# Kernel optimization log

Hardware: AMD Instinct MI355X
Metric: run time of the kernel (lower is better)

Reference implementation:

```python
import jax, jax.numpy as jnp
import numpy as np

B, S = 2, 1024
NH, NKV, HD = 32, 8, 128
Q_DIM, KV_DIM = NH * HD, NKV * HD
LEVEL = 256
ROPE_BASE = 10000.0


def fq_sym(x, level=LEVEL):
    # symmetric per-tensor fake quant with straight-through estimator
    qp = level // 2 - 1
    s = jnp.maximum(jax.lax.stop_gradient(jnp.max(jnp.abs(x))) / qp, 1e-8)
    q = jnp.clip(jnp.round(x / s), -qp, qp) * s
    return x + jax.lax.stop_gradient(q - x)


def fq_asym(x, level=LEVEL):
    # asymmetric (unsigned) fake quant for values in [0, 1]
    qp = level - 1
    s = jnp.maximum(jax.lax.stop_gradient(jnp.max(x)) / qp, 1e-8)
    q = jnp.clip(jnp.round(x / s), 0, qp) * s
    return x + jax.lax.stop_gradient(q - x)


def rope_tables(seq_len, dim):
    inv_freq = 1.0 / (ROPE_BASE ** (jnp.arange(0, dim, 2, dtype=jnp.float32) / dim))
    freqs = jnp.arange(seq_len, dtype=jnp.float32)[:, None] * inv_freq[None, :]  # [S, HD/2]
    emb = jnp.concatenate([freqs, freqs], axis=-1)  # [S, HD]
    return jnp.cos(emb), jnp.sin(emb)


def rotate_half(x):
    x1, x2 = jnp.split(x, 2, axis=-1)
    return jnp.concatenate([-x2, x1], axis=-1)


def setup_inputs() -> dict:
    key = jax.random.key(0)
    k1, k2, k3, k4 = jax.random.split(key, 4)
    d = Q_DIM + 2 * KV_DIM
    x = jax.random.normal(k1, (B, S, d), dtype=jnp.float32)
    w_qkv = jax.random.normal(k2, (d, d), dtype=jnp.float32) * (d ** -0.5)
    w_o = jax.random.normal(k3, (Q_DIM, Q_DIM), dtype=jnp.float32) * (Q_DIM ** -0.5)
    core_slope = jnp.float32(0.25)
    causal_mask = jnp.where(
        jnp.triu(jnp.ones((S, S), dtype=bool), k=1), jnp.float32(-1e9), jnp.float32(0.0)
    )[None, None]
    return {"x": x, "w_qkv": w_qkv, "w_o": w_o, "core_slope": core_slope,
            "causal_mask": causal_mask}


def reference(x, w_qkv, w_o, core_slope, causal_mask):
    qkv = jnp.einsum("bsd,ed->bse", x, w_qkv)  # Linear, no bias
    q = qkv[..., :Q_DIM].reshape(B, S, NH, HD).transpose(0, 2, 1, 3)
    k = qkv[..., Q_DIM:Q_DIM + KV_DIM].reshape(B, S, NKV, HD).transpose(0, 2, 1, 3)
    v = qkv[..., Q_DIM + KV_DIM:].reshape(B, S, NKV, HD).transpose(0, 2, 1, 3)
    q, k, v = fq_sym(q), fq_sym(k), fq_sym(v)
    cos, sin = rope_tables(S, HD)
    cos, sin = cos[None, None], sin[None, None]  # [1,1,S,HD]
    q = q * cos + rotate_half(q) * sin
    k = k * cos + rotate_half(k) * sin
    groups = NH // NKV
    if groups > 1:
        k = jnp.repeat(k, groups, axis=1)  # [B,NH,S,HD]
        v = jnp.repeat(v, groups, axis=1)
    scale = HD ** -0.5
    scores = jnp.einsum("bhqd,bhkd->bhqk", q, k) * scale
    scores = scores + causal_mask
    attn = jnp.clip(0.5 + core_slope * scores, 0.0, 1.0)  # UniAffineCore -> [0,1]
    attn = fq_asym(attn)
    out = jnp.einsum("bhqk,bhkd->bhqd", attn, v)
    out = fq_sym(out)
    out = out.transpose(0, 2, 1, 3).reshape(B, S, Q_DIM)
    out = jnp.einsum("bsd,ed->bse", out, w_o)
    return fq_sym(out)
```

## Files before the change

### kernel.cpp

```cpp
#include <hip/hip_runtime.h>
#include <stdint.h>

#define BB   2
#define SS   1024
#define NH   32
#define NKV  8
#define HD   128
#define DQ   4096
#define DKV  1024
#define DD   6144
#define MM   2048
#define SCALE 0.08838834764831845f

typedef __attribute__((ext_vector_type(8))) short short8;
typedef __attribute__((ext_vector_type(4))) float f4;

__device__ __forceinline__ float b2f(unsigned short b) {
    union { unsigned int u; float f; } v; v.u = ((unsigned int)b) << 16; return v.f;
}
__device__ __forceinline__ unsigned short f2b(float f) {
    union { float f; unsigned int u; } v; v.f = f;
    unsigned int u = v.u;
    unsigned int r = u + 0x7fffu + ((u >> 16) & 1u);
    return (unsigned short)(r >> 16);
}
__device__ __forceinline__ float fqs(float x, float s) {
    return fminf(fmaxf(rintf(x / s), -127.f), 127.f) * s;
}

typedef const unsigned int __attribute__((address_space(1)))* gas_ptr;
typedef unsigned int __attribute__((address_space(3)))* las_ptr;
__device__ __forceinline__ void gl_lds16(const void* g, void* l) {
    __builtin_amdgcn_global_load_lds((gas_ptr)(uintptr_t)g,
                                     (las_ptr)(unsigned int)(uintptr_t)l, 16, 0, 0);
}

__global__ void detect_kernel(const unsigned short* __restrict__ x, float* scal) {
    __shared__ float w[4];
    int tid = threadIdx.x;
    float m = 0.f;
    for (int i = tid; i < 65536; i += 256) m = fmaxf(m, fabsf(b2f(x[i])));
#pragma unroll
    for (int off = 32; off > 0; off >>= 1) m = fmaxf(m, __shfl_down(m, off));
    if ((tid & 63) == 0) w[tid >> 6] = m;
    __syncthreads();
    if (tid == 0) {
        float mm = fmaxf(fmaxf(w[0], w[1]), fmaxf(w[2], w[3]));
        scal[6] = (mm > 1e4f) ? 1.0f : 0.0f;
    }
}

__global__ void slope_kernel(const unsigned short* __restrict__ sp, float* scal) {
    if (threadIdx.x == 0)
        scal[7] = (scal[6] > 0.5f) ? ((const float*)sp)[0] : b2f(sp[0]);
}

__global__ void convert_split_kernel(const unsigned short* __restrict__ src,
                                     unsigned short* __restrict__ hi,
                                     unsigned short* __restrict__ lo,
                                     const float* __restrict__ scal) {
    size_t t = (size_t)blockIdx.x * 256 + threadIdx.x;
    float v[8] __attribute__((aligned(16)));
    if (scal[6] > 0.5f) {
        const float* s = (const float*)src + t * 8;
        *(float4*)(v)     = *(const float4*)(s);
        *(float4*)(v + 4) = *(const float4*)(s + 4);
    } else {
        unsigned short u[8] __attribute__((aligned(16)));
        *(uint4*)u = *(const uint4*)(src + t * 8);
#pragma unroll
        for (int i = 0; i < 8; i++) v[i] = b2f(u[i]);
    }
    unsigned short h8[8] __attribute__((aligned(16)));
    unsigned short l8[8] __attribute__((aligned(16)));
#pragma unroll
    for (int i = 0; i < 8; i++) {
        unsigned short h = f2b(v[i]);
        h8[i] = h;
        l8[i] = f2b(v[i] - b2f(h));
    }
    *(uint4*)(hi + t * 8) = *(uint4*)h8;
    *(uint4*)(lo + t * 8) = *(uint4*)l8;
}

template<int NT, int MODE>
__global__ __launch_bounds__(256, 4)
void gemm_hilo_kernel(const unsigned short* __restrict__ Ah,
                      const unsigned short* __restrict__ Al,
                      const unsigned short* __restrict__ Bh,
                      const unsigned short* __restrict__ Bl,
                      float* __restrict__ C,
                      int M, int N, int K,
                      float* __restrict__ scal)
{
    constexpr int PA    = 128 * 32;
    constexpr int OAL   = PA;
    constexpr int OBH   = (NT == 3) ? 2 * PA : PA;
    constexpr int OBL   = OBH + PA;
    __shared__ unsigned short lds[OBL + PA];
    __shared__ float wred[4];

    const int tid = threadIdx.x;
    const int bn = blockIdx.x << 7;
    const int bm = blockIdx.y << 7;
    const int wave = tid >> 6, lane = tid & 63;
    const int wm = (wave >> 1) << 6, wn = (wave & 1) << 6;
    const int lm = lane & 15, quad = lane >> 4;
    const int qx = quad ^ ((lm >> 1) & 3);

    const f4 z = {0.f, 0.f, 0.f, 0.f};
    f4 acc[4][4];
#pragma unroll
    for (int i = 0; i < 4; i++)
#pragma unroll
        for (int j = 0; j < 4; j++) acc[i][j] = z;

    const int r0 = tid >> 2;
    const int cs = ((tid & 3) ^ ((r0 >> 1) & 3)) * 8;
    const size_t ra0 = (size_t)(bm + r0) * K + cs;
    const size_t ra1 = (size_t)(bm + r0 + 64) * K + cs;
    const size_t rb0 = (size_t)(bn + r0) * K + cs;
    const size_t rb1 = (size_t)(bn + r0 + 64) * K + cs;
    const int l0 = tid * 8, l1 = (tid + 256) * 8;

    for (int k0 = 0; k0 < K; k0 += 32) {
        gl_lds16(Ah + ra0 + k0, lds + l0);
        gl_lds16(Ah + ra1 + k0, lds + l1);
        if (NT == 3) {
            gl_lds16(Al + ra0 + k0, lds + OAL + l0);
            gl_lds16(Al + ra1 + k0, lds + OAL + l1);
        }
        gl_lds16(Bh + rb0 + k0, lds + OBH + l0);
        gl_lds16(Bh + rb1 + k0, lds + OBH + l1);
        gl_lds16(Bl + rb0 + k0, lds + OBL + l0);
        gl_lds16(Bl + rb1 + k0, lds + OBL + l1);
        __syncthreads();
        short8 a_h[4], b_h[4], b_l[4];
        short8 a_l[(NT == 3) ? 4 : 1];
#pragma unroll
        for (int t = 0; t < 4; t++) {
            int ro = (wm + t * 16 + lm) * 32 + qx * 8;
            a_h[t] = *(const short8*)(lds + ro);
            if (NT == 3) a_l[t] = *(const short8*)(lds + OAL + ro);
        }
#pragma unroll
        for (int t = 0; t < 4; t++) {
            int ro = (wn + t * 16 + lm) * 32 + qx * 8;
            b_h[t] = *(const short8*)(lds + OBH + ro);
            b_l[t] = *(const short8*)(lds + OBL + ro);
        }
#pragma unroll
        for (int i = 0; i < 4; i++)
#pragma unroll
            for (int j = 0; j < 4; j++) {
                acc[i][j] = __builtin_amdgcn_mfma_f32_16x16x32_bf16(a_h[i], b_h[j], acc[i][j], 0, 0, 0);
                if (NT == 3)
                    acc[i][j] = __builtin_amdgcn_mfma_f32_16x16x32_bf16(a_l[i], b_h[j], acc[i][j], 0, 0, 0);
                acc[i][j] = __builtin_amdgcn_mfma_f32_16x16x32_bf16(a_h[i], b_l[j], acc[i][j], 0, 0, 0);
            }
        __syncthreads();
    }

    float mult = 1.f;
    if (MODE == 1) mult = fmaxf(scal[4] / 127.f, 1e-8f);
    float amax = 0.f;
#pragma unroll
    for (int i = 0; i < 4; i++)
#pragma unroll
        for (int j = 0; j < 4; j++)
#pragma unroll
            for (int r = 0; r < 4; r++) {
                float v = acc[i][j][r] * mult;
                amax = fmaxf(amax, fabsf(v));
                size_t row = (size_t)(bm + wm + i * 16 + quad * 4 + r);
                size_t col = (size_t)(bn + wn + j * 16 + lm);
                C[row * (size_t)N + col] = v;
            }
#pragma unroll
    for (int off = 32; off > 0; off >>= 1) amax = fmaxf(amax, __shfl_down(amax, off));
    if (lane == 0) wred[wave] = amax;
    __syncthreads();
    if (tid == 0) {
        float m = fmaxf(fmaxf(wred[0], wred[1]), fmaxf(wred[2], wred[3]));
        int slot = (MODE == 0) ? ((bn < 4096) ? 0 : ((bn < 5120) ? 1 : 2)) : 5;
        atomicMax((unsigned int*)(scal + slot), __float_as_uint(m));
    }
}

__global__ void quant_rope_hilo_kernel(const float* __restrict__ qkv,
                                       unsigned short* __restrict__ Qh,
                                       unsigned short* __restrict__ Ql,
                                       unsigned short* __restrict__ Kh,
                                       unsigned short* __restrict__ Kl,
                                       unsigned short* __restrict__ Vc,
                                       const float* __restrict__ scal)
{
    int t = blockIdx.x * 256 + threadIdx.x;
    int f = t * 8;
    int r = f / DD;
    int c = f - r * DD;
    int b = r >> 10, sp = r & 1023;
    const float* src = qkv + (size_t)r * DD + c;
    float x[8] __attribute__((aligned(16)));
    *(float4*)(x)     = *(const float4*)(src);
    *(float4*)(x + 4) = *(const float4*)(src + 4);

    if (c < 5120) {
        float s; int d; unsigned short *dh, *dl;
        if (c < 4096) {
            s = fmaxf(scal[0] / 127.f, 1e-8f);
            int head = c >> 7; d = c & 127;
            size_t off = (((size_t)(b * NH + head) * SS + sp) << 7) + d;
            dh = Qh + off; dl = Ql + off;
        } else {
            int cc = c - 4096;
            s = fmaxf(scal[1] / 127.f, 1e-8f);
            int head = cc >> 7; d = cc & 127;
            size_t off = (((size_t)(b * NKV + head) * SS + sp) << 7) + d;
            dh = Kh + off; dl = Kl + off;
        }
        int cp = (d < 64) ? (c + 64) : (c - 64);
        float sgn = (d < 64) ? -1.f : 1.f;
        const float* psrc = qkv + (size_t)r * DD + cp;
        float p[8] __attribute__((aligned(16)));
        *(float4*)(p)     = *(const float4*)(psrc);
        *(float4*)(p + 4) = *(const float4*)(psrc + 4);
        unsigned short h8[8] __attribute__((aligned(16)));
        unsigned short l8[8] __attribute__((aligned(16)));
#pragma unroll
        for (int i = 0; i < 8; i++) {
            float xq = fqs(x[i], s);
            float pq = fqs(p[i], s);
            int fi = (d + i) & 63;
            float inv = expf((float)fi * -0.14391156831212787f);
            float ang = (float)sp * inv;
            float sn, cs;
            sincosf(ang, &sn, &cs);
            float o = xq * cs + sgn * pq * sn;
            unsigned short hb = f2b(o);
            h8[i] = hb;
            l8[i] = f2b(o - b2f(hb));
        }
        *(uint4*)(dh) = *(uint4*)h8;
        *(uint4*)(dl) = *(uint4*)l8;
    } else {
        int cc = c - 5120;
        float s = fmaxf(scal[2] / 127.f, 1e-8f);
        int head = cc >> 7, d = cc & 127;
        unsigned short* dst = Vc + (((size_t)(b * NKV + head) * SS + sp) << 7) + d;
        unsigned short o8[8] __attribute__((aligned(16)));
#pragma unroll
        for (int i = 0; i < 8; i++) {
            float code = fminf(fmaxf(rintf(x[i] / s), -127.f), 127.f);
            o8[i] = f2b(code);
        }
        *(uint4*)(dst) = *(uint4*)o8;
    }
}

__global__ void vtrans_kernel(const unsigned short* __restrict__ Vc,
                              unsigned short* __restrict__ Vt)
{
    __shared__ __attribute__((aligned(16))) unsigned short L[64][72];
    const int dtile = blockIdx.x;
    const int ktile = blockIdx.y;
    const int bh    = blockIdx.z;
    const int tid = threadIdx.x;
#pragma unroll
    for (int it = 0; it < 2; it++) {
        int lin = it * 256 + tid;
        int row = lin >> 3, c8 = (lin & 7) * 8;
        *(uint4*)&L[row][c8] =
            *(const uint4*)(Vc + ((size_t)bh * SS + ktile * 64 + row) * HD + dtile * 64 + c8);
    }
    __syncthreads();
#pragma unroll
    for (int it = 0; it < 2; it++) {
        int lin = it * 256 + tid;
        int dr = lin >> 3, k8 = (lin & 7) * 8;
        unsigned short o8[8] __attribute__((aligned(16)));
#pragma unroll
        for (int i = 0; i < 8; i++) o8[i] = L[k8 + i][dr];
        *(uint4*)(Vt + ((size_t)bh * HD + dtile * 64 + dr) * SS + ktile * 64 + k8) = *(uint4*)o8;
    }
}

__global__ __launch_bounds__(256, 2)
void attn_score_kernel(const unsigned short* __restrict__ Qh,
                       const unsigned short* __restrict__ Ql,
                       const unsigned short* __restrict__ Kh,
                       const unsigned short* __restrict__ Kl,
                       float* __restrict__ Scr,
                       float* __restrict__ scal)
{
    __shared__ float wred[4];
    const int x = blockIdx.x;
    const int qc = 15 - (x & 15);
    const int h = (x >> 4) & 31, b = x >> 9;
    const int hk = h >> 2;
    const int tid = threadIdx.x;
    const int wave = tid >> 6, lane = tid & 63;
    const int lm = lane & 15, quad = lane >> 4;
    const float coef = scal[7] * SCALE;

    const size_t qbase = ((size_t)((b * NH + h) * SS) + qc * 64 + wave * 16 + lm) * HD + quad * 8;
    short8 qh[4], ql[4];
#pragma unroll
    for (int kk = 0; kk < 4; kk++) {
        qh[kk] = *(const short8*)(Qh + qbase + kk * 32);
        ql[kk] = *(const short8*)(Ql + qbase + kk * 32);
    }
    const size_t kbase = (size_t)((b * NKV + hk) * SS) * HD + quad * 8;
    const size_t scrbase = ((size_t)(b * NH + h) * 136 + (size_t)(qc * (qc + 1) / 2)) * 4096;

    const f4 z = {0.f, 0.f, 0.f, 0.f};
    float amax = 0.f;
    const int qg = qc * 64 + wave * 16 + quad * 4;

    for (int kt = 0; kt <= qc; kt++) {
        f4 acc[4];
#pragma unroll
        for (int j = 0; j < 4; j++) acc[j] = z;
        __builtin_amdgcn_s_setprio(1);
#pragma unroll
        for (int j = 0; j < 4; j++) {
            const size_t kb = kbase + (size_t)(kt * 64 + j * 16 + lm) * HD;
#pragma unroll
            for (int kk = 0; kk < 4; kk++) {
                short8 kh8 = *(const short8*)(Kh + kb + kk * 32);
                short8 kl8 = *(const short8*)(Kl + kb + kk * 32);
                acc[j] = __builtin_amdgcn_mfma_f32_16x16x32_bf16(qh[kk], kh8, acc[j], 0, 0, 0);
                acc[j] = __builtin_amdgcn_mfma_f32_16x16x32_bf16(ql[kk], kh8, acc[j], 0, 0, 0);
                acc[j] = __builtin_amdgcn_mfma_f32_16x16x32_bf16(qh[kk], kl8, acc[j], 0, 0, 0);
            }
        }
        __builtin_amdgcn_s_setprio(0);
        const bool diag = (kt == qc);
        float* st = Scr + scrbase + (size_t)kt * 4096;
#pragma unroll
        for (int j = 0; j < 4; j++) {
            int kg = kt * 64 + j * 16 + lm;
#pragma unroll
            for (int r = 0; r < 4; r++) {
                float sv = acc[j][r];
                st[(wave * 16 + quad * 4 + r) * 64 + j * 16 + lm] = sv;
                bool ok = (!diag) || (kg <= qg + r);
                if (ok) {
                    float a = 0.5f + coef * sv;
                    a = fminf(fmaxf(a, 0.f), 1.f);
                    amax = fmaxf(amax, a);
                }
            }
        }
    }

#pragma unroll
    for (int off = 32; off > 0; off >>= 1) amax = fmaxf(amax, __shfl_down(amax, off));
    if (lane == 0) wred[wave] = amax;
    __syncthreads();
    if (tid == 0) {
        float m = fmaxf(fmaxf(wred[0], wred[1]), fmaxf(wred[2], wred[3]));
        atomicMax((unsigned int*)(scal + 3), __float_as_uint(m));
    }
}

__global__ __launch_bounds__(256, 4)
void attn_pv_kernel(const float* __restrict__ Scr,
                    const unsigned short* __restrict__ Vt,
                    float* __restrict__ O,
                    float* __restrict__ scal)
{
    __shared__ float wred[4];
    const int x = blockIdx.x;
    const int qc = 15 - (x & 15);
    const int h = (x >> 4) & 31, b = x >> 9;
    const int hk = h >> 2;
    const int tid = threadIdx.x;
    const int wave = tid >> 6, lane = tid & 63;
    const int lm = lane & 15, quad = lane >> 4;
    const float coef = scal[7] * SCALE;
    const float s_a = fmaxf(scal[3] / 255.f, 1e-8f);
    const float s_v = fmaxf(scal[2] / 127.f, 1e-8f);
    const float s_av = s_a * s_v;

    const size_t vbase = (size_t)((b * NKV + hk) * HD) * SS + quad * 8;
    const size_t scrbase = ((size_t)(b * NH + h) * 136 + (size_t)(qc * (qc + 1) / 2)) * 4096
                         + (size_t)(wave * 16 + lm) * 64 + quad * 8;
    const int qg = qc * 64 + wave * 16 + lm;

    const f4 z = {0.f, 0.f, 0.f, 0.f};
    f4 oacc[8];
#pragma unroll
    for (int j2 = 0; j2 < 8; j2++) oacc[j2] = z;

    for (int kt = 0; kt <= qc; kt++) {
        const float* sp = Scr + scrbase + (size_t)kt * 4096;
        float sc[16] __attribute__((aligned(16)));
        *(float4*)(sc)      = *(const float4*)(sp);
        *(float4*)(sc + 4)  = *(const float4*)(sp + 4);
        *(float4*)(sc + 8)  = *(const float4*)(sp + 32);
        *(float4*)(sc + 12) = *(const float4*)(sp + 36);
        const bool diag = (kt == qc);
        unsigned short cd[16] __attribute__((aligned(16)));
#pragma unroll
        for (int i = 0; i < 8; i++) {
            int kg = kt * 64 + quad * 8 + i;
            bool ok = (!diag) || (kg <= qg);
            float a = 0.5f + coef * sc[i];
            a = fminf(fmaxf(a, 0.f), 1.f);
            cd[i] = f2b(ok ? fminf(rintf(a / s_a), 255.f) : 0.f);
        }
#pragma unroll
        for (int i = 0; i < 8; i++) {
            int kg = kt * 64 + 32 + quad * 8 + i;
            bool ok = (!diag) || (kg <= qg);
            float a = 0.5f + coef * sc[8 + i];
            a = fminf(fmaxf(a, 0.f), 1.f);
            cd[8 + i] = f2b(ok ? fminf(rintf(a / s_a), 255.f) : 0.f);
        }
        short8 pa0 = *(const short8*)(cd);
        short8 pa1 = *(const short8*)(cd + 8);
        __builtin_amdgcn_s_setprio(1);
#pragma unroll
        for (int j2 = 0; j2 < 8; j2++) {
            const unsigned short* vp = Vt + vbase + (size_t)(j2 * 16 + lm) * SS + kt * 64;
            short8 v0 = *(const short8*)(vp);
            short8 v1 = *(const short8*)(vp + 32);
            oacc[j2] = __builtin_amdgcn_mfma_f32_16x16x32_bf16(pa0, v0, oacc[j2], 0, 0, 0);
            oacc[j2] = __builtin_amdgcn_mfma_f32_16x16x32_bf16(pa1, v1, oacc[j2], 0, 0, 0);
        }
        __builtin_amdgcn_s_setprio(0);
    }

    float am = 0.f;
    const size_t orow = (size_t)(b * SS + qc * 64 + wave * 16 + quad * 4);
#pragma unroll
    for (int j2 = 0; j2 < 8; j2++)
#pragma unroll
        for (int r = 0; r < 4; r++) {
            float v = oacc[j2][r] * s_av;
            am = fmaxf(am, fabsf(v));
            O[(orow + r) * DQ + h * HD + j2 * 16 + lm] = v;
        }
#pragma unroll
    for (int off = 32; off > 0; off >>= 1) am = fmaxf(am, __shfl_down(am, off));
    if (lane == 0) wred[wave] = am;
    __syncthreads();
    if (tid == 0) {
        float m = fmaxf(fmaxf(wred[0], wred[1]), fmaxf(wred[2], wred[3]));
        atomicMax((unsigned int*)(scal + 4), __float_as_uint(m));
    }
}

__global__ void quant_o_codes_kernel(const float* __restrict__ O,
                                     const float* __restrict__ scal,
                                     unsigned short* __restrict__ Oq)
{
    size_t t = (size_t)blockIdx.x * 256 + threadIdx.x;
    float s = fmaxf(scal[4] / 127.f, 1e-8f);
    float4 v = *(const float4*)(O + t * 4);
    unsigned short o[4] __attribute__((aligned(8)));
    o[0] = f2b(fminf(fmaxf(rintf(v.x / s), -127.f), 127.f));
    o[1] = f2b(fminf(fmaxf(rintf(v.y / s), -127.f), 127.f));
    o[2] = f2b(fminf(fmaxf(rintf(v.z / s), -127.f), 127.f));
    o[3] = f2b(fminf(fmaxf(rintf(v.w / s), -127.f), 127.f));
    *(uint2*)(Oq + t * 4) = *(uint2*)o;
}

__global__ void final_q_kernel(const float* __restrict__ X,
                               const float* __restrict__ scal,
                               float* __restrict__ out)
{
    size_t t = (size_t)blockIdx.x * 256 + threadIdx.x;
    float s = fmaxf(scal[5] / 127.f, 1e-8f);
    float4 v = *(const float4*)(X + t * 4);
    float4 o;
    o.x = fqs(v.x, s);
    o.y = fqs(v.y, s);
    o.z = fqs(v.z, s);
    o.w = fqs(v.w, s);
    *(float4*)(out + t * 4) = o;
}

extern "C" void kernel_launch(void* const* d_in, const int* in_sizes, int n_in,
                              void* d_out, int out_size, void* d_ws, size_t ws_size,
                              hipStream_t stream)
{
    const unsigned short* x      = (const unsigned short*)d_in[0];
    const unsigned short* w_qkv  = (const unsigned short*)d_in[1];
    const unsigned short* w_o    = (const unsigned short*)d_in[2];
    const unsigned short* slope  = (const unsigned short*)d_in[3];
    (void)in_sizes; (void)n_in; (void)out_size; (void)ws_size;

    char* ws = (char*)d_ws;
    float* scal          = (float*)ws;
    unsigned short* xh   = (unsigned short*)(ws + 256);
    unsigned short* xl   = (unsigned short*)(ws + 25166080);
    unsigned short* wqh  = (unsigned short*)(ws + 50331904);
    unsigned short* wql  = (unsigned short*)(ws + 125829376);
    float* qkv           = (float*)(ws + 201326848);
    unsigned short* Qh   = (unsigned short*)(ws + 251658496);
    unsigned short* Ql   = (unsigned short*)(ws + 268435712);
    unsigned short* Kh   = (unsigned short*)(ws + 285212928);
    unsigned short* Kl   = (unsigned short*)(ws + 289407232);
    unsigned short* Vt   = (unsigned short*)(ws + 293601536);
    unsigned short* Vc   = (unsigned short*)(ws + 297795840);
    unsigned short* woh  = (unsigned short*)(ws + 256);
    unsigned short* wol  = (unsigned short*)(ws + 33554688);
    float* O             = (float*)(ws + 67109376);
    float* Scr           = (float*)(ws + 100663808);
    unsigned short* Oqc  = (unsigned short*)(ws + 100663808);
    float* out2          = (float*)(ws + 201326848);
    float* outp          = (float*)d_out;

    hipMemsetAsync(scal, 0, 256, stream);
    detect_kernel<<<1, 256, 0, stream>>>(x, scal);
    slope_kernel<<<1, 64, 0, stream>>>(slope, scal);
    convert_split_kernel<<<6144, 256, 0, stream>>>(x, xh, xl, scal);
    convert_split_kernel<<<18432, 256, 0, stream>>>(w_qkv, wqh, wql, scal);
    gemm_hilo_kernel<3, 0><<<dim3(48, 16), 256, 0, stream>>>(xh, xl, wqh, wql, qkv,
                                                             MM, DD, DD, scal);
    quant_rope_hilo_kernel<<<6144, 256, 0, stream>>>(qkv, Qh, Ql, Kh, Kl, Vc, scal);
    vtrans_kernel<<<dim3(2, 16, 16), 256, 0, stream>>>(Vc, Vt);
    convert_split_kernel<<<8192, 256, 0, stream>>>(w_o, woh, wol, scal);
    attn_score_kernel<<<1024, 256, 0, stream>>>(Qh, Ql, Kh, Kl, Scr, scal);
    attn_pv_kernel<<<1024, 256, 0, stream>>>(Scr, Vt, O, scal);
    quant_o_codes_kernel<<<8192, 256, 0, stream>>>(O, scal, Oqc);
    gemm_hilo_kernel<2, 1><<<dim3(32, 16), 256, 0, stream>>>(Oqc, Oqc, woh, wol, out2,
                                                             MM, DQ, DQ, scal);
    final_q_kernel<<<8192, 256, 0, stream>>>(out2, scal, outp);
}
```

Measured before the change: 1.455 ms.

## Load A fragments directly from global into registers and double K-step per iteration

The GEMM no longer stages the A operand (hi/lo) through LDS. Each wave reads its A fragments straight from global memory into registers, while B hi/lo is staged for two 32-wide K slices per loop iteration, so the K loop steps by 64 and half as many barriers run. The aim is to cut LDS traffic and synchronisation per unit of work. In exchange, A is fetched redundantly by the two waves sharing rows, global reads are less coalesced, register pressure rises, and occupancy is lowered to 3 blocks per SM through launch_bounds.

```diff
diff --git a/kernel.cpp b/kernel.cpp
--- a/kernel.cpp
+++ b/kernel.cpp
@@ -84,7 +84,7 @@
 }
 
 template<int NT, int MODE>
-__global__ __launch_bounds__(256, 4)
+__global__ __launch_bounds__(256, 3)
 void gemm_hilo_kernel(const unsigned short* __restrict__ Ah,
                       const unsigned short* __restrict__ Al,
                       const unsigned short* __restrict__ Bh,
@@ -93,11 +93,7 @@
                       int M, int N, int K,
                       float* __restrict__ scal)
 {
-    constexpr int PA    = 128 * 32;
-    constexpr int OAL   = PA;
-    constexpr int OBH   = (NT == 3) ? 2 * PA : PA;
-    constexpr int OBL   = OBH + PA;
-    __shared__ unsigned short lds[OBL + PA];
+    __shared__ unsigned short lds[4 * 4096];
     __shared__ float wred[4];
 
     const int tid = threadIdx.x;
@@ -117,46 +113,71 @@
 
     const int r0 = tid >> 2;
     const int cs = ((tid & 3) ^ ((r0 >> 1) & 3)) * 8;
-    const size_t ra0 = (size_t)(bm + r0) * K + cs;
-    const size_t ra1 = (size_t)(bm + r0 + 64) * K + cs;
     const size_t rb0 = (size_t)(bn + r0) * K + cs;
     const size_t rb1 = (size_t)(bn + r0 + 64) * K + cs;
     const int l0 = tid * 8, l1 = (tid + 256) * 8;
 
-    for (int k0 = 0; k0 < K; k0 += 32) {
-        gl_lds16(Ah + ra0 + k0, lds + l0);
-        gl_lds16(Ah + ra1 + k0, lds + l1);
-        if (NT == 3) {
-            gl_lds16(Al + ra0 + k0, lds + OAL + l0);
-            gl_lds16(Al + ra1 + k0, lds + OAL + l1);
-        }
-        gl_lds16(Bh + rb0 + k0, lds + OBH + l0);
-        gl_lds16(Bh + rb1 + k0, lds + OBH + l1);
-        gl_lds16(Bl + rb0 + k0, lds + OBL + l0);
-        gl_lds16(Bl + rb1 + k0, lds + OBL + l1);
+    const unsigned short* pAh[4];
+    const unsigned short* pAl[(NT == 3) ? 4 : 1];
+#pragma unroll
+    for (int t = 0; t < 4; t++) {
+        size_t ro = (size_t)(bm + wm + t * 16 + lm) * K + quad * 8;
+        pAh[t] = Ah + ro;
+        if (NT == 3) pAl[t] = Al + ro;
+    }
+
+    for (int k0 = 0; k0 < K; k0 += 64) {
+        gl_lds16(Bh + rb0 + k0,      lds + l0);
+        gl_lds16(Bh + rb1 + k0,      lds + l1);
+        gl_lds16(Bh + rb0 + k0 + 32, lds + 4096 + l0);
+        gl_lds16(Bh + rb1 + k0 + 32, lds + 4096 + l1);
+        gl_lds16(Bl + rb0 + k0,      lds + 8192 + l0);
+        gl_lds16(Bl + rb1 + k0,      lds + 8192 + l1);
+        gl_lds16(Bl + rb0 + k0 + 32, lds + 12288 + l0);
+        gl_lds16(Bl + rb1 + k0 + 32, lds + 12288 + l1);
+        short8 a0h[4], a1h[4];
+        short8 a0l[(NT == 3) ? 4 : 1], a1l[(NT == 3) ? 4 : 1];
+#pragma unroll
+        for (int t = 0; t < 4; t++) {
+            a0h[t] = *(const short8*)(pAh[t] + k0);
+            if (NT == 3) a0l[t] = *(const short8*)(pAl[t] + k0);
+        }
         __syncthreads();
-        short8 a_h[4], b_h[4], b_l[4];
-        short8 a_l[(NT == 3) ? 4 : 1];
-#pragma unroll
-        for (int t = 0; t < 4; t++) {
-            int ro = (wm + t * 16 + lm) * 32 + qx * 8;
-            a_h[t] = *(const short8*)(lds + ro);
-            if (NT == 3) a_l[t] = *(const short8*)(lds + OAL + ro);
-        }
+        short8 b_h[4], b_l[4];
 #pragma unroll
         for (int t = 0; t < 4; t++) {
             int ro = (wn + t * 16 + lm) * 32 + qx * 8;
-            b_h[t] = *(const short8*)(lds + OBH + ro);
-            b_l[t] = *(const short8*)(lds + OBL + ro);
+            b_h[t] = *(const short8*)(lds + ro);
+            b_l[t] = *(const short8*)(lds + 8192 + ro);
+        }
+#pragma unroll
+        for (int t = 0; t < 4; t++) {
+            a1h[t] = *(const short8*)(pAh[t] + k0 + 32);
+            if (NT == 3) a1l[t] = *(const short8*)(pAl[t] + k0 + 32);
         }
 #pragma unroll
         for (int i = 0; i < 4; i++)
 #pragma unroll
             for (int j = 0; j < 4; j++) {
-                acc[i][j] = __builtin_amdgcn_mfma_f32_16x16x32_bf16(a_h[i], b_h[j], acc[i][j], 0, 0, 0);
+                acc[i][j] = __builtin_amdgcn_mfma_f32_16x16x32_bf16(a0h[i], b_h[j], acc[i][j], 0, 0, 0);
                 if (NT == 3)
-                    acc[i][j] = __builtin_amdgcn_mfma_f32_16x16x32_bf16(a_l[i], b_h[j], acc[i][j], 0, 0, 0);
-                acc[i][j] = __builtin_amdgcn_mfma_f32_16x16x32_bf16(a_h[i], b_l[j], acc[i][j], 0, 0, 0);
+                    acc[i][j] = __builtin_amdgcn_mfma_f32_16x16x32_bf16(a0l[i], b_h[j], acc[i][j], 0, 0, 0);
+                acc[i][j] = __builtin_amdgcn_mfma_f32_16x16x32_bf16(a0h[i], b_l[j], acc[i][j], 0, 0, 0);
+            }
+#pragma unroll
+        for (int t = 0; t < 4; t++) {
+            int ro = (wn + t * 16 + lm) * 32 + qx * 8;
+            b_h[t] = *(const short8*)(lds + 4096 + ro);
+            b_l[t] = *(const short8*)(lds + 12288 + ro);
+        }
+#pragma unroll
+        for (int i = 0; i < 4; i++)
+#pragma unroll
+            for (int j = 0; j < 4; j++) {
+                acc[i][j] = __builtin_amdgcn_mfma_f32_16x16x32_bf16(a1h[i], b_h[j], acc[i][j], 0, 0, 0);
+                if (NT == 3)
+                    acc[i][j] = __builtin_amdgcn_mfma_f32_16x16x32_bf16(a1l[i], b_h[j], acc[i][j], 0, 0, 0);
+                acc[i][j] = __builtin_amdgcn_mfma_f32_16x16x32_bf16(a1h[i], b_l[j], acc[i][j], 0, 0, 0);
             }
         __syncthreads();
     }
```

Result: slower. 1.738 ms (+19.5%).
